# Kernel tuning notes

Hardware: AMD Instinct MI355X
Metric: run time of the kernel (lower is better)

The kernel has to match this reference:

```python
import jax, jax.numpy as jnp
import numpy as np

DIM = 512
HEADS = 8
D_HEAD = 64
INNER_FF = 4 * DIM  # 2048
EPS = 1e-5
SCALE = D_HEAD ** -0.5


def _layernorm(x, w, b):
    x = x.astype(jnp.float32)
    mu = jnp.mean(x, axis=-1, keepdims=True)
    var = jnp.mean(jnp.square(x - mu), axis=-1, keepdims=True)
    return (x - mu) * jax.lax.rsqrt(var + EPS) * w + b


def _l2_attn(x, wq, bq, wv, bv, wo, bo):
    # x: [B, N, DIM]. k = q (context is ignored in the original module).
    b, n, _ = x.shape
    q = (x @ wq + bq).reshape(b, n, HEADS, D_HEAD).transpose(0, 2, 1, 3)  # b h n d
    v = (x @ wv + bv).reshape(b, n, HEADS, D_HEAD).transpose(0, 2, 1, 3)
    q = q.astype(jnp.float32)
    AB = jnp.einsum('bhid,bhjd->bhij', q, q)          # [b,h,n,n]
    AA = jnp.sum(jnp.square(q), axis=-1)               # [b,h,n]
    sim = -(AA[..., :, None] - 2.0 * AB + AA[..., None, :]) * SCALE
    attn = jax.nn.softmax(sim, axis=-1)
    out = jnp.einsum('bhij,bhjd->bhid', attn, v)       # [b,h,n,d]
    out = out.transpose(0, 2, 1, 3).reshape(b, n, HEADS * D_HEAD)
    return out @ wo + bo


def _geglu_ff(x, w1, b1, w2, b2):
    h = x @ w1 + b1                      # [B, N, 2*INNER_FF]
    a, gate = jnp.split(h, 2, axis=-1)
    return (a * jax.nn.gelu(gate, approximate=False)) @ w2 + b2


def setup_inputs() -> dict:
    key = jax.random.key(0)
    ks = jax.random.split(key, 24)
    s = 0.02
    d = {'x': jax.random.normal(ks[0], (4, 2048, DIM), jnp.float32)}
    # layernorms
    d['sa_norm_w'] = jnp.ones((DIM,), jnp.float32)
    d['sa_norm_b'] = jnp.zeros((DIM,), jnp.float32)
    d['ca_norm_w'] = jnp.ones((DIM,), jnp.float32)
    d['ca_norm_b'] = jnp.zeros((DIM,), jnp.float32)
    d['ff_norm_w'] = jnp.ones((DIM,), jnp.float32)
    d['ff_norm_b'] = jnp.zeros((DIM,), jnp.float32)
    # attn1 (self)
    d['a1_wq'] = jax.random.normal(ks[1], (DIM, DIM), jnp.float32) * s
    d['a1_bq'] = jnp.zeros((DIM,), jnp.float32)
    d['a1_wv'] = jax.random.normal(ks[2], (DIM, DIM), jnp.float32) * s
    d['a1_bv'] = jnp.zeros((DIM,), jnp.float32)
    d['a1_wo'] = jax.random.normal(ks[3], (DIM, DIM), jnp.float32) * s
    d['a1_bo'] = jnp.zeros((DIM,), jnp.float32)
    # attn2 (cross, but k=q and v from x in original code)
    d['a2_wq'] = jax.random.normal(ks[4], (DIM, DIM), jnp.float32) * s
    d['a2_bq'] = jnp.zeros((DIM,), jnp.float32)
    d['a2_wv'] = jax.random.normal(ks[5], (DIM, DIM), jnp.float32) * s
    d['a2_bv'] = jnp.zeros((DIM,), jnp.float32)
    d['a2_wo'] = jax.random.normal(ks[6], (DIM, DIM), jnp.float32) * s
    d['a2_bo'] = jnp.zeros((DIM,), jnp.float32)
    # GEGLU FFN
    d['ff_w1'] = jax.random.normal(ks[7], (DIM, 2 * INNER_FF), jnp.float32) * s
    d['ff_b1'] = jnp.zeros((2 * INNER_FF,), jnp.float32)
    d['ff_w2'] = jax.random.normal(ks[8], (INNER_FF, DIM), jnp.float32) * s
    d['ff_b2'] = jnp.zeros((DIM,), jnp.float32)
    return d


def reference(x, sa_norm_w, sa_norm_b, ca_norm_w, ca_norm_b, ff_norm_w, ff_norm_b,
              a1_wq, a1_bq, a1_wv, a1_bv, a1_wo, a1_bo,
              a2_wq, a2_bq, a2_wv, a2_bv, a2_wo, a2_bo,
              ff_w1, ff_b1, ff_w2, ff_b2):
    x = _l2_attn(_layernorm(x, sa_norm_w, sa_norm_b), a1_wq, a1_bq, a1_wv, a1_bv, a1_wo, a1_bo) + x
    x = _l2_attn(_layernorm(x, ca_norm_w, ca_norm_b), a2_wq, a2_bq, a2_wv, a2_bv, a2_wo, a2_bo) + x
    x = _geglu_ff(_layernorm(x, ff_norm_w, ff_norm_b), ff_w1, ff_b1, ff_w2, ff_b2) + x
    return x
```

## Files before the change

kernel.cpp:

```cpp
#include <hip/hip_runtime.h>
#include <hip/hip_bf16.h>


typedef short bf16x8 __attribute__((ext_vector_type(8)));
typedef float f32x4 __attribute__((ext_vector_type(4)));
typedef unsigned short u16;
typedef unsigned int u32;

__device__ __forceinline__ float bf2f(u16 u) {
    return __uint_as_float(((u32)u) << 16);
}
__device__ __forceinline__ u16 f2bf(float f) {
    u32 u = __float_as_uint(f);
    u32 rb = ((u >> 16) & 1u) + 0x7fffu;
    return (u16)((u + rb) >> 16);
}
__device__ __forceinline__ float gelu_exact(float x) {
    return 0.5f * x * (1.f + erff(x * 0.7071067811865475f));
}
__device__ __forceinline__ void gl2lds16(const u16* g, u16* l) {
    __builtin_amdgcn_global_load_lds(
        (const __attribute__((address_space(1))) void*)(unsigned long long)(uintptr_t)g,
        (__attribute__((address_space(3))) void*)(unsigned long long)(uintptr_t)l,
        16, 0, 0);
}

__global__ __launch_bounds__(256) void transpose_f32_bf16(const float* __restrict__ in,
                                                          u16* __restrict__ out,
                                                          int R, int C) {
    __shared__ float tile[32][33];
    int bx = blockIdx.x, by = blockIdx.y;
    int t = threadIdx.x;
    int c = t & 31, r0 = (t >> 5) * 4;
#pragma unroll
    for (int i = 0; i < 4; i++)
        tile[r0 + i][c] = in[(size_t)(by * 32 + r0 + i) * C + bx * 32 + c];
    __syncthreads();
#pragma unroll
    for (int i = 0; i < 4; i++)
        out[(size_t)(bx * 32 + r0 + i) * R + by * 32 + c] = f2bf(tile[c][r0 + i]);
}

__global__ __launch_bounds__(256) void ln_kernel(const float* __restrict__ x,
                                                 const float* __restrict__ w,
                                                 const float* __restrict__ b,
                                                 u16* __restrict__ out) {
    int row = blockIdx.x, t = threadIdx.x;
    const float* xr = x + (size_t)row * 512;
    float2 v = *(const float2*)(xr + t * 2);
    float s1 = v.x + v.y;
    float s2 = v.x * v.x + v.y * v.y;
#pragma unroll
    for (int m = 1; m < 64; m <<= 1) {
        s1 += __shfl_xor(s1, m);
        s2 += __shfl_xor(s2, m);
    }
    __shared__ float r1[4], r2[4];
    int wave = t >> 6, lane = t & 63;
    if (lane == 0) { r1[wave] = s1; r2[wave] = s2; }
    __syncthreads();
    float tot1 = r1[0] + r1[1] + r1[2] + r1[3];
    float tot2 = r2[0] + r2[1] + r2[2] + r2[3];
    float mu = tot1 * (1.f / 512.f);
    float var = tot2 * (1.f / 512.f) - mu * mu;
    float rs = rsqrtf(var + 1e-5f);
    float2 wv = *(const float2*)(w + t * 2);
    float2 bv = *(const float2*)(b + t * 2);
    float o0 = (v.x - mu) * rs * wv.x + bv.x;
    float o1 = (v.y - mu) * rs * wv.y + bv.y;
    u32 pack = (u32)f2bf(o0) | ((u32)f2bf(o1) << 16);
    *(u32*)(out + (size_t)row * 512 + t * 2) = pack;
}

template <int MODE>
__global__ __launch_bounds__(256) void gemm128(const u16* __restrict__ A,
                                               const u16* __restrict__ BT,
                                               const float* __restrict__ bias,
                                               u16* __restrict__ outb,
                                               int M, int N, int K) {
    __shared__ u16 As[2][128 * 32];
    __shared__ u16 Bs[2][128 * 32];
    int t = threadIdx.x;
    int wave = t >> 6, lane = t & 63, quad = lane >> 4, l16 = lane & 15;
    int m0 = blockIdx.x * 128, n0 = blockIdx.y * 128;
    int wm = (wave >> 1) * 64, wn = (wave & 1) * 64;
    f32x4 acc[4][4];
#pragma unroll
    for (int i = 0; i < 4; i++)
#pragma unroll
        for (int j = 0; j < 4; j++) acc[i][j] = (f32x4){0.f, 0.f, 0.f, 0.f};
    const u16* Ag = A + (size_t)(m0 + wave * 32 + (lane >> 2)) * K + (lane & 3) * 8;
    const u16* Bg = BT + (size_t)(n0 + wave * 32 + (lane >> 2)) * K + (lane & 3) * 8;
    int lo = wave * 32 * 32;
    const size_t rstep = (size_t)16 * K;
    gl2lds16(Ag, &As[0][lo]);
    gl2lds16(Ag + rstep, &As[0][lo + 16 * 32]);
    gl2lds16(Bg, &Bs[0][lo]);
    gl2lds16(Bg + rstep, &Bs[0][lo + 16 * 32]);
    int buf = 0;
    for (int k0 = 0; k0 < K; k0 += 32, buf ^= 1) {
        int kn = (k0 + 32 < K) ? (k0 + 32) : k0;
        int nb = buf ^ 1;
        asm volatile("s_waitcnt lgkmcnt(0)\n\ts_barrier" ::: "memory");
        gl2lds16(Ag + kn, &As[nb][lo]);
        gl2lds16(Ag + kn + rstep, &As[nb][lo + 16 * 32]);
        gl2lds16(Bg + kn, &Bs[nb][lo]);
        gl2lds16(Bg + kn + rstep, &Bs[nb][lo + 16 * 32]);
        asm volatile("s_waitcnt vmcnt(4)\n\ts_barrier" ::: "memory");
        bf16x8 a[4], b[4];
#pragma unroll
        for (int i = 0; i < 4; i++) {
            a[i] = *(const bf16x8*)&As[buf][(wm + i * 16 + l16) * 32 + quad * 8];
            b[i] = *(const bf16x8*)&Bs[buf][(wn + i * 16 + l16) * 32 + quad * 8];
        }
#pragma unroll
        for (int i = 0; i < 4; i++)
#pragma unroll
            for (int j = 0; j < 4; j++)
                acc[i][j] = __builtin_amdgcn_mfma_f32_16x16x32_bf16(a[i], b[j], acc[i][j], 0, 0, 0);
    }
    asm volatile("s_waitcnt vmcnt(0)" ::: "memory");
    int row_base = m0 + wm + quad * 4;
    int col_base = n0 + wn + l16;
#pragma unroll
    for (int j = 0; j < 4; j++) {
        int col = col_base + j * 16;
        float bv = bias[col];
#pragma unroll
        for (int i = 0; i < 4; i++) {
#pragma unroll
            for (int r = 0; r < 4; r++) {
                int row = row_base + i * 16 + r;
                outb[(size_t)row * N + col] = f2bf(acc[i][j][r] + bv);
            }
        }
    }
}

template <int MODE>
__global__ __launch_bounds__(256) void gemm_rect(const u16* __restrict__ A,
                                                 const u16* __restrict__ BT,
                                                 const float* __restrict__ bias,
                                                 const float* __restrict__ bias2,
                                                 const float* __restrict__ res,
                                                 float* __restrict__ outf,
                                                 u16* __restrict__ outb,
                                                 u16* __restrict__ outb2,
                                                 int M, int N, int K) {
    __shared__ u16 As[2][128 * 32];
    __shared__ u16 Bs[2][64 * 32];
    int t = threadIdx.x;
    int wave = t >> 6, lane = t & 63, quad = lane >> 4, l16 = lane & 15;
    int m0 = blockIdx.x * 128, n0 = blockIdx.y * 64;
    f32x4 acc[2][4];
#pragma unroll
    for (int i = 0; i < 2; i++)
#pragma unroll
        for (int j = 0; j < 4; j++) acc[i][j] = (f32x4){0.f, 0.f, 0.f, 0.f};
    const u16* Ag = A + (size_t)(m0 + wave * 32 + (lane >> 2)) * K + (lane & 3) * 8;
    const u16* Bg = BT + (size_t)(n0 + wave * 16 + (lane >> 2)) * K + (lane & 3) * 8;
    int loA = wave * 32 * 32;
    int loB = wave * 16 * 32;
    const size_t rstep = (size_t)16 * K;
    gl2lds16(Ag, &As[0][loA]);
    gl2lds16(Ag + rstep, &As[0][loA + 16 * 32]);
    gl2lds16(Bg, &Bs[0][loB]);
    int buf = 0;
    for (int k0 = 0; k0 < K; k0 += 32, buf ^= 1) {
        int kn = (k0 + 32 < K) ? (k0 + 32) : k0;
        int nb = buf ^ 1;
        asm volatile("s_waitcnt lgkmcnt(0)\n\ts_barrier" ::: "memory");
        gl2lds16(Ag + kn, &As[nb][loA]);
        gl2lds16(Ag + kn + rstep, &As[nb][loA + 16 * 32]);
        gl2lds16(Bg + kn, &Bs[nb][loB]);
        asm volatile("s_waitcnt vmcnt(3)\n\ts_barrier" ::: "memory");
        bf16x8 a[2], b[4];
#pragma unroll
        for (int i = 0; i < 2; i++)
            a[i] = *(const bf16x8*)&As[buf][(wave * 32 + i * 16 + l16) * 32 + quad * 8];
#pragma unroll
        for (int j = 0; j < 4; j++)
            b[j] = *(const bf16x8*)&Bs[buf][(j * 16 + l16) * 32 + quad * 8];
#pragma unroll
        for (int i = 0; i < 2; i++)
#pragma unroll
            for (int j = 0; j < 4; j++)
                acc[i][j] = __builtin_amdgcn_mfma_f32_16x16x32_bf16(a[i], b[j], acc[i][j], 0, 0, 0);
    }
    asm volatile("s_waitcnt vmcnt(0)" ::: "memory");
    int row_base = m0 + wave * 32 + quad * 4;
#pragma unroll
    for (int j = 0; j < 4; j++) {
        int col = n0 + j * 16 + l16;
        float bv;
        if (MODE == 4) bv = (col < 512) ? bias[col] : bias2[col - 512];
        else bv = bias[col];
#pragma unroll
        for (int i = 0; i < 2; i++) {
            int rowA = row_base + i * 16;
            if (MODE == 4) {
                if (col < 512) {
                    int hh = col >> 6, d = col & 63;
#pragma unroll
                    for (int r = 0; r < 4; r++) {
                        int row = rowA + r;
                        outb[((size_t)((row >> 11) * 8 + hh) * 2048 + (row & 2047)) * 64 + d] =
                            f2bf(acc[i][j][r] + bv);
                    }
                } else {
                    int c2 = col - 512;
                    int hh = c2 >> 6, d = c2 & 63;
                    int n = rowA & 2047;
                    int a4 = (n >> 2) & 7;
                    int ncol = (n & ~31) + ((a4 & 3) << 3) + ((a4 >> 2) << 2);
                    u32 plo = (u32)f2bf(acc[i][j][0] + bv) | ((u32)f2bf(acc[i][j][1] + bv) << 16);
                    u32 phi = (u32)f2bf(acc[i][j][2] + bv) | ((u32)f2bf(acc[i][j][3] + bv) << 16);
                    uint2 pk; pk.x = plo; pk.y = phi;
                    *(uint2*)&outb2[((size_t)((rowA >> 11) * 8 + hh) * 64 + d) * 2048 + ncol] = pk;
                }
            } else {
#pragma unroll
                for (int r = 0; r < 4; r++) {
                    size_t idx = (size_t)(rowA + r) * N + col;
                    outf[idx] = acc[i][j][r] + bv + res[idx];
                }
            }
        }
    }
}

__global__ __launch_bounds__(256) void aa_kernel(const u16* __restrict__ q,
                                                 float* __restrict__ aa) {
    int t = threadIdx.x;
    int tok = blockIdx.x * 32 + (t >> 3);
    int l8 = t & 7;
    const u16* row = q + (size_t)tok * 64 + l8 * 8;
    uint4 u = *(const uint4*)row;
    u32 c[4] = {u.x, u.y, u.z, u.w};
    float s = 0.f;
#pragma unroll
    for (int k = 0; k < 4; k++) {
        float a = bf2f((u16)(c[k] & 0xffff));
        float b = bf2f((u16)(c[k] >> 16));
        s += a * a + b * b;
    }
    s += __shfl_xor(s, 1); s += __shfl_xor(s, 2); s += __shfl_xor(s, 4);
    if (l8 == 0) aa[tok] = s * 0.125f;
}

__global__ __launch_bounds__(256) void attn_mfma(const u16* __restrict__ qbuf,
                                                 const u16* __restrict__ vtp,
                                                 const float* __restrict__ aas,
                                                 u16* __restrict__ out) {
    __shared__ u16 Qj[64][72];
    __shared__ u16 VT[64][72];
    int itile = blockIdx.x, bh = blockIdx.y;
    const u16* qb = qbuf + (size_t)bh * 2048 * 64;
    const u16* vtb = vtp + (size_t)bh * 64 * 2048;
    const float* aab = aas + (size_t)bh * 2048;
    int t = threadIdx.x;
    int wave = t >> 6, lane = t & 63, quad = lane >> 4, l16 = lane & 15;
    int ibase = itile * 64 + wave * 16;
    bf16x8 qf0 = *(const bf16x8*)(qb + (size_t)(ibase + l16) * 64 + quad * 8);
    bf16x8 qf1 = *(const bf16x8*)(qb + (size_t)(ibase + l16) * 64 + 32 + quad * 8);
    float ci = aab[ibase + l16];
    f32x4 O[4];
#pragma unroll
    for (int nt = 0; nt < 4; nt++) O[nt] = (f32x4){0.f, 0.f, 0.f, 0.f};
    float lr = 0.f;
    int sr = t >> 2, sc = (t & 3) * 16;
    uint4 nq0, nq1, nv0, nv1;
    {
        const u16* srcq = qb + (size_t)sr * 64 + sc;
        nq0 = *(const uint4*)srcq;
        nq1 = *(const uint4*)(srcq + 8);
        const u16* srcv = vtb + (size_t)sr * 2048 + sc;
        nv0 = *(const uint4*)srcv;
        nv1 = *(const uint4*)(srcv + 8);
    }
    for (int j0 = 0; j0 < 2048; j0 += 64) {
        __syncthreads();
        *(uint4*)&Qj[sr][sc] = nq0;
        *(uint4*)&Qj[sr][sc + 8] = nq1;
        *(uint4*)&VT[sr][sc] = nv0;
        *(uint4*)&VT[sr][sc + 8] = nv1;
        if (j0 + 64 < 2048) {
            const u16* srcq = qb + (size_t)(j0 + 64 + sr) * 64 + sc;
            nq0 = *(const uint4*)srcq;
            nq1 = *(const uint4*)(srcq + 8);
            const u16* srcv = vtb + (size_t)sr * 2048 + (j0 + 64) + sc;
            nv0 = *(const uint4*)srcv;
            nv1 = *(const uint4*)(srcv + 8);
        }
        __syncthreads();
#pragma unroll
        for (int c = 0; c < 2; c++) {
            int j1 = c * 32, j2 = c * 32 + 16;
            bf16x8 a10 = *(const bf16x8*)&Qj[j1 + l16][quad * 8];
            bf16x8 a11 = *(const bf16x8*)&Qj[j1 + l16][32 + quad * 8];
            f32x4 s0 = {0.f, 0.f, 0.f, 0.f};
            s0 = __builtin_amdgcn_mfma_f32_16x16x32_bf16(a10, qf0, s0, 0, 0, 0);
            s0 = __builtin_amdgcn_mfma_f32_16x16x32_bf16(a11, qf1, s0, 0, 0, 0);
            bf16x8 a20 = *(const bf16x8*)&Qj[j2 + l16][quad * 8];
            bf16x8 a21 = *(const bf16x8*)&Qj[j2 + l16][32 + quad * 8];
            f32x4 s1 = {0.f, 0.f, 0.f, 0.f};
            s1 = __builtin_amdgcn_mfma_f32_16x16x32_bf16(a20, qf0, s1, 0, 0, 0);
            s1 = __builtin_amdgcn_mfma_f32_16x16x32_bf16(a21, qf1, s1, 0, 0, 0);
            float4 aav0 = *(const float4*)(aab + j0 + j1 + quad * 4);
            float4 aav1 = *(const float4*)(aab + j0 + j2 + quad * 4);
            float p0 = __expf(s0[0] * 0.25f - aav0.x - ci);
            float p1 = __expf(s0[1] * 0.25f - aav0.y - ci);
            float p2 = __expf(s0[2] * 0.25f - aav0.z - ci);
            float p3 = __expf(s0[3] * 0.25f - aav0.w - ci);
            float p4 = __expf(s1[0] * 0.25f - aav1.x - ci);
            float p5 = __expf(s1[1] * 0.25f - aav1.y - ci);
            float p6 = __expf(s1[2] * 0.25f - aav1.z - ci);
            float p7 = __expf(s1[3] * 0.25f - aav1.w - ci);
            lr += (p0 + p1 + p2 + p3) + (p4 + p5 + p6 + p7);
            bf16x8 pa;
            pa[0] = (short)f2bf(p0); pa[1] = (short)f2bf(p1);
            pa[2] = (short)f2bf(p2); pa[3] = (short)f2bf(p3);
            pa[4] = (short)f2bf(p4); pa[5] = (short)f2bf(p5);
            pa[6] = (short)f2bf(p6); pa[7] = (short)f2bf(p7);
#pragma unroll
            for (int nt = 0; nt < 4; nt++) {
                bf16x8 vf = *(const bf16x8*)&VT[nt * 16 + l16][c * 32 + quad * 8];
                O[nt] = __builtin_amdgcn_mfma_f32_16x16x32_bf16(pa, vf, O[nt], 0, 0, 0);
            }
        }
    }
    lr += __shfl_xor(lr, 16);
    lr += __shfl_xor(lr, 32);
    float inv = 1.f / lr;
    int b = bh >> 3, h = bh & 7;
#pragma unroll
    for (int r = 0; r < 4; r++) {
        float invr = __shfl(inv, quad * 4 + r);
        size_t row = (size_t)(b * 2048 + ibase + quad * 4 + r);
        u16* o = out + row * 512 + h * 64 + l16;
        o[0]  = f2bf(O[0][r] * invr);
        o[16] = f2bf(O[1][r] * invr);
        o[32] = f2bf(O[2][r] * invr);
        o[48] = f2bf(O[3][r] * invr);
    }
}

__global__ __launch_bounds__(256) void geglu_kernel(const u16* __restrict__ h,
                                                    u16* __restrict__ g) {
    size_t i = ((size_t)blockIdx.x * 256 + threadIdx.x) * 4;
    size_t m = i >> 11;
    int c = (int)(i & 2047);
    const u16* p = h + m * 4096 + c;
    uint2 ua = *(const uint2*)p;
    uint2 ug = *(const uint2*)(p + 2048);
    float a0 = bf2f((u16)(ua.x & 0xffff)), a1 = bf2f((u16)(ua.x >> 16));
    float a2 = bf2f((u16)(ua.y & 0xffff)), a3 = bf2f((u16)(ua.y >> 16));
    float g0 = bf2f((u16)(ug.x & 0xffff)), g1 = bf2f((u16)(ug.x >> 16));
    float g2 = bf2f((u16)(ug.y & 0xffff)), g3 = bf2f((u16)(ug.y >> 16));
    float r0 = a0 * gelu_exact(g0);
    float r1 = a1 * gelu_exact(g1);
    float r2 = a2 * gelu_exact(g2);
    float r3 = a3 * gelu_exact(g3);
    uint2 o;
    o.x = (u32)f2bf(r0) | ((u32)f2bf(r1) << 16);
    o.y = (u32)f2bf(r2) | ((u32)f2bf(r3) << 16);
    *(uint2*)(g + m * 2048 + c) = o;
}

extern "C" void kernel_launch(void* const* d_in, const int* in_sizes, int n_in,
                              void* d_out, int out_size, void* d_ws, size_t ws_size,
                              hipStream_t stream) {
    const float* x      = (const float*)d_in[0];
    const float* sa_w   = (const float*)d_in[1];
    const float* sa_b   = (const float*)d_in[2];
    const float* ca_w   = (const float*)d_in[3];
    const float* ca_b   = (const float*)d_in[4];
    const float* ffn_w  = (const float*)d_in[5];
    const float* ffn_b  = (const float*)d_in[6];
    const float* a1_wq  = (const float*)d_in[7];
    const float* a1_bq  = (const float*)d_in[8];
    const float* a1_wv  = (const float*)d_in[9];
    const float* a1_bv  = (const float*)d_in[10];
    const float* a1_wo  = (const float*)d_in[11];
    const float* a1_bo  = (const float*)d_in[12];
    const float* a2_wq  = (const float*)d_in[13];
    const float* a2_bq  = (const float*)d_in[14];
    const float* a2_wv  = (const float*)d_in[15];
    const float* a2_bv  = (const float*)d_in[16];
    const float* a2_wo  = (const float*)d_in[17];
    const float* a2_bo  = (const float*)d_in[18];
    const float* ff_w1  = (const float*)d_in[19];
    const float* ff_b1  = (const float*)d_in[20];
    const float* ff_w2  = (const float*)d_in[21];
    const float* ff_b2  = (const float*)d_in[22];

    char* ws = (char*)d_ws;
    const size_t MB = 1ull << 20;
    float* x_res   = (float*)(ws);
    u16* xn        = (u16*)(ws + 16 * MB);
    u16* wT_a1qv   = (u16*)(ws + 24 * MB);
    u16* wT_a2qv   = (u16*)(ws + 25 * MB);
    u16* wT_a1o    = (u16*)(ws + 26 * MB);
    u16* wT_a2o    = (u16*)(ws + 26 * MB + 512 * 1024);
    u16* wT_ff1    = (u16*)(ws + 27 * MB);
    u16* wT_ff2    = (u16*)(ws + 31 * MB);
    u16* qbuf      = (u16*)(ws + 34 * MB);
    u16* vtp       = (u16*)(ws + 42 * MB);
    float* aab     = (float*)(ws + 50 * MB);
    u16* attn_o    = (u16*)(ws + 51 * MB);
    u16* hbuf      = (u16*)(ws + 34 * MB);
    u16* gbuf      = (u16*)(ws + 98 * MB);

    (void)in_sizes; (void)n_in; (void)out_size; (void)ws_size;

    transpose_f32_bf16<<<dim3(16, 16), 256, 0, stream>>>(a1_wq, wT_a1qv, 512, 512);
    transpose_f32_bf16<<<dim3(16, 16), 256, 0, stream>>>(a1_wv, wT_a1qv + 512 * 512, 512, 512);
    transpose_f32_bf16<<<dim3(16, 16), 256, 0, stream>>>(a2_wq, wT_a2qv, 512, 512);
    transpose_f32_bf16<<<dim3(16, 16), 256, 0, stream>>>(a2_wv, wT_a2qv + 512 * 512, 512, 512);
    transpose_f32_bf16<<<dim3(16, 16), 256, 0, stream>>>(a1_wo, wT_a1o, 512, 512);
    transpose_f32_bf16<<<dim3(16, 16), 256, 0, stream>>>(a2_wo, wT_a2o, 512, 512);
    transpose_f32_bf16<<<dim3(128, 16), 256, 0, stream>>>(ff_w1, wT_ff1, 512, 4096);
    transpose_f32_bf16<<<dim3(16, 64), 256, 0, stream>>>(ff_w2, wT_ff2, 2048, 512);

    ln_kernel<<<8192, 256, 0, stream>>>(x, sa_w, sa_b, xn);
    gemm_rect<4><<<dim3(64, 16), 256, 0, stream>>>(xn, wT_a1qv, a1_bq, a1_bv, nullptr, nullptr, qbuf, vtp, 8192, 1024, 512);
    aa_kernel<<<2048, 256, 0, stream>>>(qbuf, aab);
    attn_mfma<<<dim3(32, 32), 256, 0, stream>>>(qbuf, vtp, aab, attn_o);
    gemm_rect<2><<<dim3(64, 8), 256, 0, stream>>>(attn_o, wT_a1o, a1_bo, nullptr, x, x_res, nullptr, nullptr, 8192, 512, 512);

    ln_kernel<<<8192, 256, 0, stream>>>(x_res, ca_w, ca_b, xn);
    gemm_rect<4><<<dim3(64, 16), 256, 0, stream>>>(xn, wT_a2qv, a2_bq, a2_bv, nullptr, nullptr, qbuf, vtp, 8192, 1024, 512);
    aa_kernel<<<2048, 256, 0, stream>>>(qbuf, aab);
    attn_mfma<<<dim3(32, 32), 256, 0, stream>>>(qbuf, vtp, aab, attn_o);
    gemm_rect<2><<<dim3(64, 8), 256, 0, stream>>>(attn_o, wT_a2o, a2_bo, nullptr, x_res, x_res, nullptr, nullptr, 8192, 512, 512);

    ln_kernel<<<8192, 256, 0, stream>>>(x_res, ffn_w, ffn_b, xn);
    gemm128<1><<<dim3(64, 32), 256, 0, stream>>>(xn, wT_ff1, ff_b1, hbuf, 8192, 4096, 512);
    geglu_kernel<<<16384, 256, 0, stream>>>(hbuf, gbuf);
    gemm_rect<2><<<dim3(64, 8), 256, 0, stream>>>(gbuf, wT_ff2, ff_b2, nullptr, x_res, (float*)d_out, nullptr, nullptr, 8192, 512, 2048);
}
```

Baseline: 462.1 us.

## Fuse GEGLU into FF1 GEMM epilogue and row-norm into QV projection

The FF1 GEMM now loads paired value and gate weight rows into one block, keeps two accumulator sets, and applies a*gelu(gate) in the epilogue. This removes the 4096-wide intermediate write and the separate GEGLU pass. The squared-norm computation (aa_kernel) is folded into the QV projection epilogue through shuffle reductions. The probability packing in attention now uses a byte-permute truncation in place of rounding float-to-bf16 conversion, which changes the rounding slightly.

```diff
diff --git a/kernel.cpp b/kernel.cpp
--- a/kernel.cpp
+++ b/kernel.cpp
@@ -72,25 +72,27 @@
     *(u32*)(out + (size_t)row * 512 + t * 2) = pack;
 }
 
-template <int MODE>
-__global__ __launch_bounds__(256) void gemm128(const u16* __restrict__ A,
-                                               const u16* __restrict__ BT,
-                                               const float* __restrict__ bias,
-                                               u16* __restrict__ outb,
-                                               int M, int N, int K) {
+__global__ __launch_bounds__(256) void gemm_ff1(const u16* __restrict__ A,
+                                                const u16* __restrict__ BT,
+                                                const float* __restrict__ bias,
+                                                u16* __restrict__ gout,
+                                                int K) {
     __shared__ u16 As[2][128 * 32];
     __shared__ u16 Bs[2][128 * 32];
     int t = threadIdx.x;
     int wave = t >> 6, lane = t & 63, quad = lane >> 4, l16 = lane & 15;
-    int m0 = blockIdx.x * 128, n0 = blockIdx.y * 128;
-    int wm = (wave >> 1) * 64, wn = (wave & 1) * 64;
-    f32x4 acc[4][4];
-#pragma unroll
-    for (int i = 0; i < 4; i++)
-#pragma unroll
-        for (int j = 0; j < 4; j++) acc[i][j] = (f32x4){0.f, 0.f, 0.f, 0.f};
+    int m0 = blockIdx.x * 128, n0 = blockIdx.y * 64;
+    f32x4 aacc[2][4], gacc[2][4];
+#pragma unroll
+    for (int i = 0; i < 2; i++)
+#pragma unroll
+        for (int j = 0; j < 4; j++) {
+            aacc[i][j] = (f32x4){0.f, 0.f, 0.f, 0.f};
+            gacc[i][j] = (f32x4){0.f, 0.f, 0.f, 0.f};
+        }
     const u16* Ag = A + (size_t)(m0 + wave * 32 + (lane >> 2)) * K + (lane & 3) * 8;
-    const u16* Bg = BT + (size_t)(n0 + wave * 32 + (lane >> 2)) * K + (lane & 3) * 8;
+    int brow = (wave < 2) ? (n0 + wave * 32) : (2048 + n0 + (wave - 2) * 32);
+    const u16* Bg = BT + (size_t)(brow + (lane >> 2)) * K + (lane & 3) * 8;
     int lo = wave * 32 * 32;
     const size_t rstep = (size_t)16 * K;
     gl2lds16(Ag, &As[0][lo]);
@@ -107,31 +109,36 @@
         gl2lds16(Bg + kn, &Bs[nb][lo]);
         gl2lds16(Bg + kn + rstep, &Bs[nb][lo + 16 * 32]);
         asm volatile("s_waitcnt vmcnt(4)\n\ts_barrier" ::: "memory");
-        bf16x8 a[4], b[4];
-#pragma unroll
-        for (int i = 0; i < 4; i++) {
-            a[i] = *(const bf16x8*)&As[buf][(wm + i * 16 + l16) * 32 + quad * 8];
-            b[i] = *(const bf16x8*)&Bs[buf][(wn + i * 16 + l16) * 32 + quad * 8];
-        }
-#pragma unroll
-        for (int i = 0; i < 4; i++)
-#pragma unroll
-            for (int j = 0; j < 4; j++)
-                acc[i][j] = __builtin_amdgcn_mfma_f32_16x16x32_bf16(a[i], b[j], acc[i][j], 0, 0, 0);
+        bf16x8 a[2];
+#pragma unroll
+        for (int i = 0; i < 2; i++)
+            a[i] = *(const bf16x8*)&As[buf][(wave * 32 + i * 16 + l16) * 32 + quad * 8];
+#pragma unroll
+        for (int j = 0; j < 4; j++) {
+            bf16x8 ba = *(const bf16x8*)&Bs[buf][(j * 16 + l16) * 32 + quad * 8];
+            bf16x8 bg = *(const bf16x8*)&Bs[buf][(64 + j * 16 + l16) * 32 + quad * 8];
+#pragma unroll
+            for (int i = 0; i < 2; i++) {
+                aacc[i][j] = __builtin_amdgcn_mfma_f32_16x16x32_bf16(a[i], ba, aacc[i][j], 0, 0, 0);
+                gacc[i][j] = __builtin_amdgcn_mfma_f32_16x16x32_bf16(a[i], bg, gacc[i][j], 0, 0, 0);
+            }
+        }
     }
     asm volatile("s_waitcnt vmcnt(0)" ::: "memory");
-    int row_base = m0 + wm + quad * 4;
-    int col_base = n0 + wn + l16;
+    int row_base = m0 + wave * 32 + quad * 4;
 #pragma unroll
     for (int j = 0; j < 4; j++) {
-        int col = col_base + j * 16;
-        float bv = bias[col];
-#pragma unroll
-        for (int i = 0; i < 4; i++) {
+        int col = n0 + j * 16 + l16;
+        float ba = bias[col];
+        float bg = bias[2048 + col];
+#pragma unroll
+        for (int i = 0; i < 2; i++) {
 #pragma unroll
             for (int r = 0; r < 4; r++) {
                 int row = row_base + i * 16 + r;
-                outb[(size_t)row * N + col] = f2bf(acc[i][j][r] + bv);
+                float av = aacc[i][j][r] + ba;
+                float gv = gacc[i][j][r] + bg;
+                gout[(size_t)row * 2048 + col] = f2bf(av * gelu_exact(gv));
             }
         }
     }
@@ -146,6 +153,7 @@
                                                  float* __restrict__ outf,
                                                  u16* __restrict__ outb,
                                                  u16* __restrict__ outb2,
+                                                 float* __restrict__ aa,
                                                  int M, int N, int K) {
     __shared__ u16 As[2][128 * 32];
     __shared__ u16 Bs[2][64 * 32];
@@ -189,6 +197,11 @@
     }
     asm volatile("s_waitcnt vmcnt(0)" ::: "memory");
     int row_base = m0 + wave * 32 + quad * 4;
+    float ssq[2][4];
+#pragma unroll
+    for (int i = 0; i < 2; i++)
+#pragma unroll
+        for (int r = 0; r < 4; r++) ssq[i][r] = 0.f;
 #pragma unroll
     for (int j = 0; j < 4; j++) {
         int col = n0 + j * 16 + l16;
@@ -204,8 +217,9 @@
 #pragma unroll
                     for (int r = 0; r < 4; r++) {
                         int row = rowA + r;
-                        outb[((size_t)((row >> 11) * 8 + hh) * 2048 + (row & 2047)) * 64 + d] =
-                            f2bf(acc[i][j][r] + bv);
+                        float v = acc[i][j][r] + bv;
+                        ssq[i][r] += v * v;
+                        outb[((size_t)((row >> 11) * 8 + hh) * 2048 + (row & 2047)) * 64 + d] = f2bf(v);
                     }
                 } else {
                     int c2 = col - 512;
@@ -227,25 +241,22 @@
             }
         }
     }
-}
-
-__global__ __launch_bounds__(256) void aa_kernel(const u16* __restrict__ q,
-                                                 float* __restrict__ aa) {
-    int t = threadIdx.x;
-    int tok = blockIdx.x * 32 + (t >> 3);
-    int l8 = t & 7;
-    const u16* row = q + (size_t)tok * 64 + l8 * 8;
-    uint4 u = *(const uint4*)row;
-    u32 c[4] = {u.x, u.y, u.z, u.w};
-    float s = 0.f;
-#pragma unroll
-    for (int k = 0; k < 4; k++) {
-        float a = bf2f((u16)(c[k] & 0xffff));
-        float b = bf2f((u16)(c[k] >> 16));
-        s += a * a + b * b;
-    }
-    s += __shfl_xor(s, 1); s += __shfl_xor(s, 2); s += __shfl_xor(s, 4);
-    if (l8 == 0) aa[tok] = s * 0.125f;
+    if (MODE == 4 && n0 < 512) {
+        int hh = n0 >> 6;
+#pragma unroll
+        for (int i = 0; i < 2; i++) {
+#pragma unroll
+            for (int r = 0; r < 4; r++) {
+                float s = ssq[i][r];
+                s += __shfl_xor(s, 1); s += __shfl_xor(s, 2);
+                s += __shfl_xor(s, 4); s += __shfl_xor(s, 8);
+                if (l16 == 0) {
+                    int row = row_base + i * 16 + r;
+                    aa[(size_t)((row >> 11) * 8 + hh) * 2048 + (row & 2047)] = s * 0.125f;
+                }
+            }
+        }
+    }
 }
 
 __global__ __launch_bounds__(256) void attn_mfma(const u16* __restrict__ qbuf,
@@ -318,10 +329,11 @@
             float p7 = __expf(s1[3] * 0.25f - aav1.w - ci);
             lr += (p0 + p1 + p2 + p3) + (p4 + p5 + p6 + p7);
             bf16x8 pa;
-            pa[0] = (short)f2bf(p0); pa[1] = (short)f2bf(p1);
-            pa[2] = (short)f2bf(p2); pa[3] = (short)f2bf(p3);
-            pa[4] = (short)f2bf(p4); pa[5] = (short)f2bf(p5);
-            pa[6] = (short)f2bf(p6); pa[7] = (short)f2bf(p7);
+            u32* pu = (u32*)&pa;
+            pu[0] = __builtin_amdgcn_perm(__float_as_uint(p1), __float_as_uint(p0), 0x07060302u);
+            pu[1] = __builtin_amdgcn_perm(__float_as_uint(p3), __float_as_uint(p2), 0x07060302u);
+            pu[2] = __builtin_amdgcn_perm(__float_as_uint(p5), __float_as_uint(p4), 0x07060302u);
+            pu[3] = __builtin_amdgcn_perm(__float_as_uint(p7), __float_as_uint(p6), 0x07060302u);
 #pragma unroll
             for (int nt = 0; nt < 4; nt++) {
                 bf16x8 vf = *(const bf16x8*)&VT[nt * 16 + l16][c * 32 + quad * 8];
@@ -343,28 +355,6 @@
         o[32] = f2bf(O[2][r] * invr);
         o[48] = f2bf(O[3][r] * invr);
     }
-}
-
-__global__ __launch_bounds__(256) void geglu_kernel(const u16* __restrict__ h,
-                                                    u16* __restrict__ g) {
-    size_t i = ((size_t)blockIdx.x * 256 + threadIdx.x) * 4;
-    size_t m = i >> 11;
-    int c = (int)(i & 2047);
-    const u16* p = h + m * 4096 + c;
-    uint2 ua = *(const uint2*)p;
-    uint2 ug = *(const uint2*)(p + 2048);
-    float a0 = bf2f((u16)(ua.x & 0xffff)), a1 = bf2f((u16)(ua.x >> 16));
-    float a2 = bf2f((u16)(ua.y & 0xffff)), a3 = bf2f((u16)(ua.y >> 16));
-    float g0 = bf2f((u16)(ug.x & 0xffff)), g1 = bf2f((u16)(ug.x >> 16));
-    float g2 = bf2f((u16)(ug.y & 0xffff)), g3 = bf2f((u16)(ug.y >> 16));
-    float r0 = a0 * gelu_exact(g0);
-    float r1 = a1 * gelu_exact(g1);
-    float r2 = a2 * gelu_exact(g2);
-    float r3 = a3 * gelu_exact(g3);
-    uint2 o;
-    o.x = (u32)f2bf(r0) | ((u32)f2bf(r1) << 16);
-    o.y = (u32)f2bf(r2) | ((u32)f2bf(r3) << 16);
-    *(uint2*)(g + m * 2048 + c) = o;
 }
 
 extern "C" void kernel_launch(void* const* d_in, const int* in_sizes, int n_in,
@@ -408,8 +398,7 @@
     u16* vtp       = (u16*)(ws + 42 * MB);
     float* aab     = (float*)(ws + 50 * MB);
     u16* attn_o    = (u16*)(ws + 51 * MB);
-    u16* hbuf      = (u16*)(ws + 34 * MB);
-    u16* gbuf      = (u16*)(ws + 98 * MB);
+    u16* gbuf      = (u16*)(ws + 60 * MB);
 
     (void)in_sizes; (void)n_in; (void)out_size; (void)ws_size;
 
@@ -423,19 +412,16 @@
     transpose_f32_bf16<<<dim3(16, 64), 256, 0, stream>>>(ff_w2, wT_ff2, 2048, 512);
 
     ln_kernel<<<8192, 256, 0, stream>>>(x, sa_w, sa_b, xn);
-    gemm_rect<4><<<dim3(64, 16), 256, 0, stream>>>(xn, wT_a1qv, a1_bq, a1_bv, nullptr, nullptr, qbuf, vtp, 8192, 1024, 512);
-    aa_kernel<<<2048, 256, 0, stream>>>(qbuf, aab);
+    gemm_rect<4><<<dim3(64, 16), 256, 0, stream>>>(xn, wT_a1qv, a1_bq, a1_bv, nullptr, nullptr, qbuf, vtp, aab, 8192, 1024, 512);
     attn_mfma<<<dim3(32, 32), 256, 0, stream>>>(qbuf, vtp, aab, attn_o);
-    gemm_rect<2><<<dim3(64, 8), 256, 0, stream>>>(attn_o, wT_a1o, a1_bo, nullptr, x, x_res, nullptr, nullptr, 8192, 512, 512);
+    gemm_rect<2><<<dim3(64, 8), 256, 0, stream>>>(attn_o, wT_a1o, a1_bo, nullptr, x, x_res, nullptr, nullptr, nullptr, 8192, 512, 512);
 
     ln_kernel<<<8192, 256, 0, stream>>>(x_res, ca_w, ca_b, xn);
-    gemm_rect<4><<<dim3(64, 16), 256, 0, stream>>>(xn, wT_a2qv, a2_bq, a2_bv, nullptr, nullptr, qbuf, vtp, 8192, 1024, 512);
-    aa_kernel<<<2048, 256, 0, stream>>>(qbuf, aab);
+    gemm_rect<4><<<dim3(64, 16), 256, 0, stream>>>(xn, wT_a2qv, a2_bq, a2_bv, nullptr, nullptr, qbuf, vtp, aab, 8192, 1024, 512);
     attn_mfma<<<dim3(32, 32), 256, 0, stream>>>(qbuf, vtp, aab, attn_o);
-    gemm_rect<2><<<dim3(64, 8), 256, 0, stream>>>(attn_o, wT_a2o, a2_bo, nullptr, x_res, x_res, nullptr, nullptr, 8192, 512, 512);
+    gemm_rect<2><<<dim3(64, 8), 256, 0, stream>>>(attn_o, wT_a2o, a2_bo, nullptr, x_res, x_res, nullptr, nullptr, nullptr, 8192, 512, 512);
 
     ln_kernel<<<8192, 256, 0, stream>>>(x_res, ffn_w, ffn_b, xn);
-    gemm128<1><<<dim3(64, 32), 256, 0, stream>>>(xn, wT_ff1, ff_b1, hbuf, 8192, 4096, 512);
-    geglu_kernel<<<16384, 256, 0, stream>>>(hbuf, gbuf);
-    gemm_rect<2><<<dim3(64, 8), 256, 0, stream>>>(gbuf, wT_ff2, ff_b2, nullptr, x_res, (float*)d_out, nullptr, nullptr, 8192, 512, 2048);
-}
+    gemm_ff1<<<dim3(64, 32), 256, 0, stream>>>(xn, wT_ff1, ff_b1, gbuf, 512);
+    gemm_rect<2><<<dim3(64, 8), 256, 0, stream>>>(gbuf, wT_ff2, ff_b2, nullptr, x_res, (float*)d_out, nullptr, nullptr, nullptr, 8192, 512, 2048);
+}
```

New measurement: 428.8 us. -7.2%, faster.
